# Optimization experiments

Measured on AMD Instinct MI355X. Metric: run time of the kernel, lower is better.

Reference implementation:

```python
import jax, jax.numpy as jnp
import numpy as np

B, N, K = 4, 40960, 16
D_IN, D_OUT = 32, 64


def setup_inputs() -> dict:
    key = jax.random.key(0)
    keys = iter(jax.random.split(key, 48))
    def nrm(shape, scale):
        return (jax.random.normal(next(keys), shape, jnp.float32) * scale).astype(jnp.float32)
    inp = {
        "feature": jax.random.normal(next(keys), (B, N, D_IN), jnp.float32),
        "xyz": jax.random.uniform(next(keys), (B, N, 3), jnp.float32),
        "neigh_idx": jax.random.randint(next(keys), (B, N, K), 0, N, jnp.int32),
    }
    def conv_bn(name, cin, cout):
        inp["w_" + name] = nrm((cin, cout), (2.0 / cin) ** 0.5)
        inp["s_" + name] = 1.0 + nrm((cout,), 0.1)  # folded BN scale: gamma/sqrt(var+eps)
        inp["b_" + name] = nrm((cout,), 0.1)        # folded BN bias: beta - mean*scale
    conv_bn("mlp1", D_IN, D_OUT // 2)
    conv_bn("lfa1", 10, D_OUT // 2)
    inp["w_att1_fc"] = nrm((D_OUT, D_OUT), (2.0 / D_OUT) ** 0.5)
    conv_bn("att1_mlp", D_OUT, D_OUT // 2)
    conv_bn("lfa2", D_OUT // 2, D_OUT // 2)
    inp["w_att2_fc"] = nrm((D_OUT, D_OUT), (2.0 / D_OUT) ** 0.5)
    conv_bn("att2_mlp", D_OUT, D_OUT)
    conv_bn("mlp2", D_OUT, 2 * D_OUT)
    conv_bn("sc", D_IN, 2 * D_OUT)
    return inp


def _gather(pc, idx):
    # pc: [B,N,D], idx: [B,N,K] -> [B,N,K,D]
    b, n, k = idx.shape
    flat = jnp.take_along_axis(pc, idx.reshape(b, n * k, 1), axis=1)
    return flat.reshape(b, n, k, pc.shape[-1])


def _cb(x, w, s, b, relu=True):
    # 1x1 conv + folded BN (+ ReLU), channels-last
    y = jnp.einsum('...i,io->...o', x, w) * s + b
    return jnp.maximum(y, 0.0) if relu else y


def _att_pool(fs, w_fc, w, s, b):
    # fs: [B,N,K,C]; softmax-attention pooling over K, then mlp
    scores = jax.nn.softmax(jnp.einsum('bnkc,cd->bnkd', fs, w_fc), axis=2)
    agg = jnp.sum(fs * scores, axis=2)  # [B,N,C]
    return _cb(agg, w, s, b)


def _rel_pos(xyz, idx):
    nbr = _gather(xyz, idx)                           # [B,N,K,3]
    tile = jnp.broadcast_to(xyz[:, :, None, :], nbr.shape)
    rel = tile - nbr
    dist = jnp.sqrt(jnp.sum(rel * rel, axis=-1, keepdims=True))
    return jnp.concatenate([dist, rel, tile, nbr], axis=-1)  # [B,N,K,10]


def reference(feature, xyz, neigh_idx,
              w_mlp1, s_mlp1, b_mlp1,
              w_lfa1, s_lfa1, b_lfa1,
              w_att1_fc, w_att1_mlp, s_att1_mlp, b_att1_mlp,
              w_lfa2, s_lfa2, b_lfa2,
              w_att2_fc, w_att2_mlp, s_att2_mlp, b_att2_mlp,
              w_mlp2, s_mlp2, b_mlp2,
              w_sc, s_sc, b_sc):
    f_pc = _cb(feature, w_mlp1, s_mlp1, b_mlp1)                   # [B,N,d/2]
    f_xyz = _cb(_rel_pos(xyz, neigh_idx), w_lfa1, s_lfa1, b_lfa1)  # [B,N,K,d/2]
    f_nb = _gather(f_pc, neigh_idx)                                # [B,N,K,d/2]
    f_agg = _att_pool(jnp.concatenate([f_nb, f_xyz], axis=-1),
                      w_att1_fc, w_att1_mlp, s_att1_mlp, b_att1_mlp)  # [B,N,d/2]
    f_xyz2 = _cb(f_xyz, w_lfa2, s_lfa2, b_lfa2)                    # [B,N,K,d/2]
    f_nb2 = _gather(f_agg, neigh_idx)                              # [B,N,K,d/2]
    f_pc2 = _att_pool(jnp.concatenate([f_nb2, f_xyz2], axis=-1),
                      w_att2_fc, w_att2_mlp, s_att2_mlp, b_att2_mlp)  # [B,N,d]
    out = _cb(f_pc2, w_mlp2, s_mlp2, b_mlp2, relu=False)           # [B,N,2d]
    sc = _cb(feature, w_sc, s_sc, b_sc, relu=False)
    return jax.nn.leaky_relu(out + sc, negative_slope=0.2)
```

## Files before the change

kernel.cpp:

```cpp
#include <hip/hip_runtime.h>
#include <hip/hip_bf16.h>

#define NPTS  40960
#define BNPTS 163840
#define KNB   16

#define PK_MLP1 0
#define PK_FC1  1280
#define PK_FC2  6912
#define PK_L1   12544
#define PK_L2   13824
#define PK_M1   15104
#define PK_M2   17920
#define PK_W2   23552
#define PK_WS   34816
#define PK_TOTAL 39936

using bf16x8 = __attribute__((ext_vector_type(8))) short;
using f32x4  = __attribute__((ext_vector_type(4))) float;

__device__ __forceinline__ unsigned short f2bf(float x) {
    union { float f; unsigned u; } v; v.f = x;
    unsigned r = v.u + 0x7fffu + ((v.u >> 16) & 1u);
    return (unsigned short)(r >> 16);
}
__device__ __forceinline__ float bf2f(unsigned short u) {
    union { unsigned u; float f; } v; v.u = ((unsigned)u) << 16;
    return v.f;
}
__device__ __forceinline__ unsigned pk2(float lo, float hi) {
    union { __hip_bfloat162 h; unsigned u; } v;
    v.h = __float22bfloat162_rn(float2{lo, hi});
    return v.u;
}
__device__ __forceinline__ bf16x8 pack8(float a0, float a1, float a2, float a3,
                                        float a4, float a5, float a6, float a7) {
    union { unsigned u[4]; bf16x8 v; } w;
    w.u[0] = pk2(a0, a1); w.u[1] = pk2(a2, a3);
    w.u[2] = pk2(a4, a5); w.u[3] = pk2(a6, a7);
    return w.v;
}
__device__ __forceinline__ f32x4 mfma16(bf16x8 a, bf16x8 b, f32x4 c) {
    return __builtin_amdgcn_mfma_f32_16x16x32_bf16(a, b, c, 0, 0, 0);
}
__device__ __forceinline__ float exp2_fast(float x) { return __builtin_amdgcn_exp2f(x); }
__device__ __forceinline__ float rcp_fast(float x)  { return __builtin_amdgcn_rcpf(x); }

__global__ __launch_bounds__(256)
void k_prep(const float* __restrict__ wm1, const float* __restrict__ wfc1,
            const float* __restrict__ wfc2,
            const float* __restrict__ wlfa1, const float* __restrict__ slfa1, const float* __restrict__ blfa1,
            const float* __restrict__ wlfa2,
            const float* __restrict__ wam1, const float* __restrict__ wam2,
            const float* __restrict__ w2, const float* __restrict__ wsc,
            unsigned short* __restrict__ pk)
{
    const int tid = threadIdx.x, blk = blockIdx.x;
    const float LOG2E = 1.4426950408889634f;
    switch (blk) {
    case 0:
        for (int t = tid; t < 32 * 32; t += 256) {
            int c = t >> 5, d = t & 31;
            pk[PK_MLP1 + d * 40 + c] = f2bf(wm1[t]);
        }
        break;
    case 1:
        for (int t = tid; t < 64 * 64; t += 256) {
            int c = t >> 6, d = t & 63;
            pk[PK_FC1 + d * 88 + c] = f2bf(wfc1[t] * LOG2E);
        }
        break;
    case 2:
        for (int t = tid; t < 64 * 64; t += 256) {
            int c = t >> 6, d = t & 63;
            pk[PK_FC2 + d * 88 + c] = f2bf(wfc2[t] * LOG2E);
        }
        break;
    case 3:
        for (int t = tid; t < 32 * 32; t += 256) {
            int k = t >> 5, d = t & 31;
            int slot = (d & 1) * 16 + (d >> 1);
            float v1 = k < 10 ? wlfa1[k * 32 + d] * slfa1[d] : (k == 10 ? blfa1[d] : 0.f);
            pk[PK_L1 + slot * 40 + k] = f2bf(v1);
            pk[PK_L2 + slot * 40 + k] = f2bf(wlfa2[k * 32 + d]);
        }
        break;
    case 4:
        for (int t = tid; t < 64 * 32; t += 256) {
            int c = t / 32, d = t % 32;
            int slot = (d & 1) * 16 + (d >> 1);
            pk[PK_M1 + slot * 88 + c] = f2bf(wam1[t]);
        }
        break;
    case 5:
        for (int t = tid; t < 64 * 64; t += 256) {
            int c = t >> 6, d = t & 63;
            int slot = (d >> 5) * 32 + (d & 1) * 16 + ((d & 31) >> 1);
            pk[PK_M2 + slot * 88 + c] = f2bf(wam2[t]);
        }
        break;
    case 6:
        for (int t = tid; t < 64 * 128; t += 256) {
            int c = t >> 7, d = t & 127;
            pk[PK_W2 + d * 88 + c] = f2bf(w2[t]);
        }
        break;
    case 7:
        for (int t = tid; t < 32 * 128; t += 256) {
            int c = t >> 7, d = t & 127;
            pk[PK_WS + d * 40 + c] = f2bf(wsc[t]);
        }
        break;
    }
}

__global__ __launch_bounds__(256)
void k_mlp1(const float* __restrict__ feature, const unsigned short* __restrict__ pk,
            const float* __restrict__ s, const float* __restrict__ b,
            unsigned short* __restrict__ f_pc)
{
    const int tid = threadIdx.x;
    const int lid = tid & 63, wv = tid >> 6;
    const int col = lid & 15, quad = lid >> 4;
    bf16x8 B0 = *(const bf16x8*)&pk[PK_MLP1 + col * 40 + quad * 8];
    bf16x8 B1 = *(const bf16x8*)&pk[PK_MLP1 + (16 + col) * 40 + quad * 8];
    float s0 = s[col], b0 = b[col], s1 = s[16 + col], b1 = b[16 + col];
    for (int itp = 0; itp < 4; itp++) {
        const int p0 = blockIdx.x * 256 + wv * 64 + itp * 16;
        const float* fr = &feature[(size_t)(p0 + col) * 32 + quad * 8];
        float4 u0 = *(const float4*)fr;
        float4 u1 = *(const float4*)(fr + 4);
        bf16x8 a = pack8(u0.x, u0.y, u0.z, u0.w, u1.x, u1.y, u1.z, u1.w);
        f32x4 z = {0.f, 0.f, 0.f, 0.f};
        f32x4 d0 = mfma16(a, B0, z);
        f32x4 d1 = mfma16(a, B1, z);
        #pragma unroll
        for (int r = 0; r < 4; r++) {
            int p = p0 + quad * 4 + r;
            f_pc[(size_t)p * 32 + col]      = f2bf(fmaxf(d0[r] * s0 + b0, 0.f));
            f_pc[(size_t)p * 32 + 16 + col] = f2bf(fmaxf(d1[r] * s1 + b1, 0.f));
        }
    }
}

template<int NOUT, bool HAS_LFA2>
__global__ __launch_bounds__(256, 4)
void k_att(const float* __restrict__ xyz, const int* __restrict__ nidx,
           const unsigned short* __restrict__ src,
           const unsigned short* __restrict__ wl1T, const unsigned short* __restrict__ wl2T,
           const float* __restrict__ slfa2, const float* __restrict__ blfa2,
           const unsigned short* __restrict__ wfcT, const unsigned short* __restrict__ wmT,
           const float* __restrict__ smlp, const float* __restrict__ bmlp,
           unsigned short* __restrict__ out)
{
    constexpr int NP = NOUT / 32;
    constexpr int WS = 88;
    __shared__ __align__(16) char smem[16384];
    char* uni = smem;

    const int tid = threadIdx.x;
    const int lid = tid & 63, wv = tid >> 6;
    const int col = lid & 15, quad = lid >> 4;

    bf16x8 Bfc[4][2];
    #pragma unroll
    for (int nt = 0; nt < 4; nt++)
        #pragma unroll
        for (int ks = 0; ks < 2; ks++)
            Bfc[nt][ks] = *(const bf16x8*)&wfcT[(nt * 16 + col) * WS + ks * 32 + quad * 8];
    bf16x8 Bl1e = *(const bf16x8*)&wl1T[col * 40 + quad * 8];
    bf16x8 Bl1o = *(const bf16x8*)&wl1T[(16 + col) * 40 + quad * 8];
    bf16x8 Bl2e{}, Bl2o{};
    float sl2e = 0.f, bl2e = 0.f, sl2o = 0.f, bl2o = 0.f;
    if (HAS_LFA2) {
        Bl2e = *(const bf16x8*)&wl2T[col * 40 + quad * 8];
        Bl2o = *(const bf16x8*)&wl2T[(16 + col) * 40 + quad * 8];
        sl2e = slfa2[2 * col]; bl2e = blfa2[2 * col];
        sl2o = slfa2[2 * col + 1]; bl2o = blfa2[2 * col + 1];
    }
    float sme[NP], bme[NP], smo[NP], bmo[NP];
    #pragma unroll
    for (int tp = 0; tp < NP; tp++) {
        sme[tp] = smlp[tp * 32 + 2 * col]; bme[tp] = bmlp[tp * 32 + 2 * col];
        smo[tp] = smlp[tp * 32 + 2 * col + 1]; bmo[tp] = bmlp[tp * 32 + 2 * col + 1];
    }
    bf16x8 Bme_r[2], Bmo_r[2];
    if constexpr (NOUT == 32) {
        #pragma unroll
        for (int ks = 0; ks < 2; ks++) {
            Bme_r[ks] = *(const bf16x8*)&wmT[col * WS + ks * 32 + quad * 8];
            Bmo_r[ks] = *(const bf16x8*)&wmT[(16 + col) * WS + ks * 32 + quad * 8];
        }
    }

    unsigned short* fc  = (unsigned short*)(uni) + wv * (16 * WS);
    unsigned short* ag  = (unsigned short*)(uni + 11264) + wv * (4 * 72);
    unsigned short* nb  = (unsigned short*)(uni + 13568) + wv * 256;
    float*          cxy = (float*)(uni + 15616) + wv * 48;

    const int blk = (int)blockIdx.x;
    const int vblk = (blk & 7) * 320 + (blk >> 3);
    const int pbase = vblk * 64 + wv * 16;
    const int pb = (pbase / NPTS) * NPTS;
    const unsigned short* srcb = src + (size_t)pb * 32;
    const float* xyzb = xyz + (size_t)pb * 3;

    {
        int4 t4 = *(const int4*)&nidx[(size_t)pbase * KNB + lid * 4];
        ushort4 u = make_ushort4((unsigned short)t4.x, (unsigned short)t4.y,
                                 (unsigned short)t4.z, (unsigned short)t4.w);
        *(ushort4*)&nb[lid * 4] = u;
        if (lid < 48) cxy[lid] = xyz[(size_t)pbase * 3 + lid];
    }

    const f32x4 z = {0.f, 0.f, 0.f, 0.f};
    bf16x8 vs; float nx = 0.f, ny = 0.f, nz = 0.f;
    {
        int j = (int)nb[col];
        vs = *(const bf16x8*)(srcb + (size_t)j * 32 + quad * 8);
        if (quad < 2) { const float* xp = xyzb + (size_t)j * 3; nx = xp[0]; ny = xp[1]; nz = xp[2]; }
    }

    #pragma unroll 1
    for (int it = 0; it < 16; it++) {
        const int p = pbase + it;
        bf16x8 a0 = vs;
        *(bf16x8*)&fc[col * WS + quad * 8] = a0;

        float cx = cxy[it * 3], cy = cxy[it * 3 + 1], cz = cxy[it * 3 + 2];
        float rx = cx - nx, ry = cy - ny, rz = cz - nz;
        float dd = sqrtf(rx * rx + ry * ry + rz * rz);
        float f0 = 0.f, f1 = 0.f, f2 = 0.f, f3 = 0.f, f4 = 0.f, f5 = 0.f, f6 = 0.f, f7 = 0.f;
        if (quad == 0)      { f0 = dd; f1 = rx; f2 = ry; f3 = rz; f4 = cx; f5 = cy; f6 = cz; f7 = nx; }
        else if (quad == 1) { f0 = ny; f1 = nz; f2 = 1.0f; }
        bf16x8 al = pack8(f0, f1, f2, f3, f4, f5, f6, f7);

        {
            int itn = it < 15 ? it + 1 : 15;
            int j = (int)nb[itn * 16 + col];
            vs = *(const bf16x8*)(srcb + (size_t)j * 32 + quad * 8);
            if (quad < 2) { const float* xp = xyzb + (size_t)j * 3; nx = xp[0]; ny = xp[1]; nz = xp[2]; }
        }

        {
            f32x4 d0 = mfma16(al, Bl1e, z);
            f32x4 d1 = mfma16(al, Bl1o, z);
            #pragma unroll
            for (int r = 0; r < 4; r++) {
                float ye = fmaxf(d0[r], 0.f);
                float yo = fmaxf(d1[r], 0.f);
                *(unsigned*)&fc[(quad * 4 + r) * WS + 32 + 2 * col] = pk2(ye, yo);
            }
            if (HAS_LFA2) {
                bf16x8 a2 = *(const bf16x8*)&fc[col * WS + 32 + quad * 8];
                f32x4 e0 = mfma16(a2, Bl2e, z);
                f32x4 e1 = mfma16(a2, Bl2o, z);
                #pragma unroll
                for (int r = 0; r < 4; r++) {
                    float ye = fmaxf(e0[r] * sl2e + bl2e, 0.f);
                    float yo = fmaxf(e1[r] * sl2o + bl2o, 0.f);
                    *(unsigned*)&fc[(quad * 4 + r) * WS + 32 + 2 * col] = pk2(ye, yo);
                }
            }
        }

        {
            bf16x8 a1 = *(const bf16x8*)&fc[col * WS + 32 + quad * 8];
            #pragma unroll
            for (int nt = 0; nt < 4; nt++) {
                f32x4 L = mfma16(a1, Bfc[nt][1], mfma16(a0, Bfc[nt][0], z));
                float e0 = exp2_fast(L[0]), e1 = exp2_fast(L[1]);
                float e2 = exp2_fast(L[2]), e3 = exp2_fast(L[3]);
                float sden = (e0 + e1) + (e2 + e3);
                const unsigned short* frr = &fc[quad * 4 * WS + nt * 16 + col];
                float av = e0 * bf2f(frr[0]) + e1 * bf2f(frr[WS]) + e2 * bf2f(frr[2 * WS]) + e3 * bf2f(frr[3 * WS]);
                av   += __shfl_xor(av, 16, 64);
                sden += __shfl_xor(sden, 16, 64);
                av   += __shfl_xor(av, 32, 64);
                sden += __shfl_xor(sden, 32, 64);
                if (quad == 0) ag[(it & 3) * 72 + nt * 16 + col] = f2bf(av * rcp_fast(sden));
            }
        }

        if ((it & 3) == 3) {
            bf16x8 am0 = *(const bf16x8*)&ag[(col & 3) * 72 + quad * 8];
            bf16x8 am1 = *(const bf16x8*)&ag[(col & 3) * 72 + 32 + quad * 8];
            #pragma unroll
            for (int tp = 0; tp < NP; tp++) {
                bf16x8 Be0, Be1, Bo0, Bo1;
                if constexpr (NOUT == 32) {
                    Be0 = Bme_r[0]; Be1 = Bme_r[1];
                    Bo0 = Bmo_r[0]; Bo1 = Bmo_r[1];
                } else {
                    Be0 = *(const bf16x8*)&wmT[(tp * 32 + col) * WS + quad * 8];
                    Be1 = *(const bf16x8*)&wmT[(tp * 32 + col) * WS + 32 + quad * 8];
                    Bo0 = *(const bf16x8*)&wmT[(tp * 32 + 16 + col) * WS + quad * 8];
                    Bo1 = *(const bf16x8*)&wmT[(tp * 32 + 16 + col) * WS + 32 + quad * 8];
                }
                f32x4 de = mfma16(am1, Be1, mfma16(am0, Be0, z));
                f32x4 dq = mfma16(am1, Bo1, mfma16(am0, Bo0, z));
                if (quad == 0) {
                    #pragma unroll
                    for (int r = 0; r < 4; r++) {
                        float ye = fmaxf(de[r] * sme[tp] + bme[tp], 0.f);
                        float yo = fmaxf(dq[r] * smo[tp] + bmo[tp], 0.f);
                        *(unsigned*)&out[(size_t)(p - 3 + r) * NOUT + tp * 32 + 2 * col] = pk2(ye, yo);
                    }
                }
            }
        }
    }
}

__global__ __launch_bounds__(256)
void k_out(const unsigned short* __restrict__ f_pc2, const float* __restrict__ feature,
           const unsigned short* __restrict__ pk,
           const float* __restrict__ s2, const float* __restrict__ b2,
           const float* __restrict__ ssc, const float* __restrict__ bsc,
           float* __restrict__ out)
{
    __shared__ float sA[128], sB2[128], sC[128];
    const int tid = threadIdx.x;
    if (tid < 128) { sA[tid] = s2[tid]; sB2[tid] = ssc[tid]; sC[tid] = b2[tid] + bsc[tid]; }
    __syncthreads();
    const int lid = tid & 63, wv = tid >> 6;
    const int col = lid & 15, quad = lid >> 4;
    const unsigned short* w2T = pk + PK_W2;
    const unsigned short* wsT = pk + PK_WS;
    const f32x4 z = {0.f, 0.f, 0.f, 0.f};
    #pragma unroll 1
    for (int itp = 0; itp < 2; itp++) {
        const int p0 = blockIdx.x * 128 + wv * 32 + itp * 16;
        const unsigned short* ar = &f_pc2[(size_t)(p0 + col) * 64 + quad * 8];
        bf16x8 a10 = *(const bf16x8*)ar;
        bf16x8 a11 = *(const bf16x8*)(ar + 32);
        const float* fr = &feature[(size_t)(p0 + col) * 32 + quad * 8];
        float4 u0 = *(const float4*)fr;
        float4 u1 = *(const float4*)(fr + 4);
        bf16x8 a2 = pack8(u0.x, u0.y, u0.z, u0.w, u1.x, u1.y, u1.z, u1.w);
        #pragma unroll 2
        for (int nt = 0; nt < 8; nt++) {
            bf16x8 bk0 = *(const bf16x8*)&w2T[(nt * 16 + col) * 88 + quad * 8];
            bf16x8 bk1 = *(const bf16x8*)&w2T[(nt * 16 + col) * 88 + 32 + quad * 8];
            bf16x8 bs  = *(const bf16x8*)&wsT[(nt * 16 + col) * 40 + quad * 8];
            f32x4 d = mfma16(a11, bk1, mfma16(a10, bk0, z));
            f32x4 e = mfma16(a2, bs, z);
            int n = nt * 16 + col;
            float ss = sA[n], st = sB2[n], bb = sC[n];
            #pragma unroll
            for (int r = 0; r < 4; r++) {
                float y = d[r] * ss + e[r] * st + bb;
                y = y > 0.f ? y : 0.2f * y;
                out[(size_t)(p0 + quad * 4 + r) * 128 + n] = y;
            }
        }
    }
}

extern "C" void kernel_launch(void* const* d_in, const int* in_sizes, int n_in,
                              void* d_out, int out_size, void* d_ws, size_t ws_size,
                              hipStream_t stream) {
    const float* feature = (const float*)d_in[0];
    const float* xyz     = (const float*)d_in[1];
    const int*   nidx    = (const int*)d_in[2];
    const float* w_mlp1 = (const float*)d_in[3];
    const float* s_mlp1 = (const float*)d_in[4];
    const float* b_mlp1 = (const float*)d_in[5];
    const float* w_lfa1 = (const float*)d_in[6];
    const float* s_lfa1 = (const float*)d_in[7];
    const float* b_lfa1 = (const float*)d_in[8];
    const float* w_att1_fc  = (const float*)d_in[9];
    const float* w_att1_mlp = (const float*)d_in[10];
    const float* s_att1_mlp = (const float*)d_in[11];
    const float* b_att1_mlp = (const float*)d_in[12];
    const float* w_lfa2 = (const float*)d_in[13];
    const float* s_lfa2 = (const float*)d_in[14];
    const float* b_lfa2 = (const float*)d_in[15];
    const float* w_att2_fc  = (const float*)d_in[16];
    const float* w_att2_mlp = (const float*)d_in[17];
    const float* s_att2_mlp = (const float*)d_in[18];
    const float* b_att2_mlp = (const float*)d_in[19];
    const float* w_mlp2 = (const float*)d_in[20];
    const float* s_mlp2 = (const float*)d_in[21];
    const float* b_mlp2 = (const float*)d_in[22];
    const float* w_sc = (const float*)d_in[23];
    const float* s_sc = (const float*)d_in[24];
    const float* b_sc = (const float*)d_in[25];

    unsigned short* f_pc  = (unsigned short*)d_ws;
    unsigned short* f_agg = f_pc  + (size_t)BNPTS * 32;
    unsigned short* f_pc2 = f_agg + (size_t)BNPTS * 32;
    unsigned short* pkw   = f_pc2 + (size_t)BNPTS * 64;
    float* out = (float*)d_out;

    k_prep<<<8, 256, 0, stream>>>(w_mlp1, w_att1_fc, w_att2_fc,
                                  w_lfa1, s_lfa1, b_lfa1, w_lfa2,
                                  w_att1_mlp, w_att2_mlp, w_mlp2, w_sc, pkw);
    k_mlp1<<<BNPTS / 256, 256, 0, stream>>>(feature, pkw, s_mlp1, b_mlp1, f_pc);
    k_att<32, false><<<BNPTS / 64, 256, 0, stream>>>(
        xyz, nidx, f_pc,
        pkw + PK_L1, pkw + PK_L1,
        s_lfa1, b_lfa1,
        pkw + PK_FC1, pkw + PK_M1, s_att1_mlp, b_att1_mlp, f_agg);
    k_att<64, true><<<BNPTS / 64, 256, 0, stream>>>(
        xyz, nidx, f_agg,
        pkw + PK_L1, pkw + PK_L2,
        s_lfa2, b_lfa2,
        pkw + PK_FC2, pkw + PK_M2, s_att2_mlp, b_att2_mlp, f_pc2);
    k_out<<<BNPTS / 128, 256, 0, stream>>>(
        f_pc2, feature, pkw,
        s_mlp2, b_mlp2, s_sc, b_sc, out);
}
```

Baseline: 364.7 us.

## Interleave weight columns for paired stores and double-buffer attention LDS tile

Repacks the mlp1, mlp2 and shortcut weights so each lane computes an adjacent even/odd output pair. This lets k_mlp1 write packed 32-bit bf16 pairs and k_out write float2 stores instead of scalar ones, and it moves k_out's scale/bias from shared memory into registers. k_att now double-buffers its per-wave fc LDS tile across iterations and unrolls by two, aiming to overlap consecutive iterations. The cost is more LDS per block (27 KB instead of 16 KB), which may lower occupancy, plus more registers.

```diff
diff --git a/kernel.cpp b/kernel.cpp
--- a/kernel.cpp
+++ b/kernel.cpp
@@ -61,7 +61,8 @@
     case 0:
         for (int t = tid; t < 32 * 32; t += 256) {
             int c = t >> 5, d = t & 31;
-            pk[PK_MLP1 + d * 40 + c] = f2bf(wm1[t]);
+            int slot = (d & 1) * 16 + (d >> 1);
+            pk[PK_MLP1 + slot * 40 + c] = f2bf(wm1[t]);
         }
         break;
     case 1:
@@ -102,13 +103,15 @@
     case 6:
         for (int t = tid; t < 64 * 128; t += 256) {
             int c = t >> 7, d = t & 127;
-            pk[PK_W2 + d * 88 + c] = f2bf(w2[t]);
+            int slot = (d >> 5) * 32 + (d & 1) * 16 + ((d & 31) >> 1);
+            pk[PK_W2 + slot * 88 + c] = f2bf(w2[t]);
         }
         break;
     case 7:
         for (int t = tid; t < 32 * 128; t += 256) {
             int c = t >> 7, d = t & 127;
-            pk[PK_WS + d * 40 + c] = f2bf(wsc[t]);
+            int slot = (d >> 5) * 32 + (d & 1) * 16 + ((d & 31) >> 1);
+            pk[PK_WS + slot * 40 + c] = f2bf(wsc[t]);
         }
         break;
     }
@@ -124,7 +127,7 @@
     const int col = lid & 15, quad = lid >> 4;
     bf16x8 B0 = *(const bf16x8*)&pk[PK_MLP1 + col * 40 + quad * 8];
     bf16x8 B1 = *(const bf16x8*)&pk[PK_MLP1 + (16 + col) * 40 + quad * 8];
-    float s0 = s[col], b0 = b[col], s1 = s[16 + col], b1 = b[16 + col];
+    float s0 = s[2 * col], b0 = b[2 * col], s1 = s[2 * col + 1], b1 = b[2 * col + 1];
     for (int itp = 0; itp < 4; itp++) {
         const int p0 = blockIdx.x * 256 + wv * 64 + itp * 16;
         const float* fr = &feature[(size_t)(p0 + col) * 32 + quad * 8];
@@ -137,8 +140,9 @@
         #pragma unroll
         for (int r = 0; r < 4; r++) {
             int p = p0 + quad * 4 + r;
-            f_pc[(size_t)p * 32 + col]      = f2bf(fmaxf(d0[r] * s0 + b0, 0.f));
-            f_pc[(size_t)p * 32 + 16 + col] = f2bf(fmaxf(d1[r] * s1 + b1, 0.f));
+            float ye = fmaxf(d0[r] * s0 + b0, 0.f);
+            float yo = fmaxf(d1[r] * s1 + b1, 0.f);
+            *(unsigned*)&f_pc[(size_t)p * 32 + 2 * col] = pk2(ye, yo);
         }
     }
 }
@@ -155,7 +159,7 @@
 {
     constexpr int NP = NOUT / 32;
     constexpr int WS = 88;
-    __shared__ __align__(16) char smem[16384];
+    __shared__ __align__(16) char smem[27648];
     char* uni = smem;
 
     const int tid = threadIdx.x;
@@ -193,10 +197,10 @@
         }
     }
 
-    unsigned short* fc  = (unsigned short*)(uni) + wv * (16 * WS);
-    unsigned short* ag  = (unsigned short*)(uni + 11264) + wv * (4 * 72);
-    unsigned short* nb  = (unsigned short*)(uni + 13568) + wv * 256;
-    float*          cxy = (float*)(uni + 15616) + wv * 48;
+    unsigned short* fc  = (unsigned short*)(uni) + wv * 2816;
+    unsigned short* ag  = (unsigned short*)(uni + 22528) + wv * 288;
+    unsigned short* nb  = (unsigned short*)(uni + 24832) + wv * 256;
+    float*          cxy = (float*)(uni + 26880) + wv * 48;
 
     const int blk = (int)blockIdx.x;
     const int vblk = (blk & 7) * 320 + (blk >> 3);
@@ -221,11 +225,12 @@
         if (quad < 2) { const float* xp = xyzb + (size_t)j * 3; nx = xp[0]; ny = xp[1]; nz = xp[2]; }
     }
 
-    #pragma unroll 1
+    #pragma unroll 2
     for (int it = 0; it < 16; it++) {
         const int p = pbase + it;
+        unsigned short* fcb = fc + (it & 1) * 1408;
         bf16x8 a0 = vs;
-        *(bf16x8*)&fc[col * WS + quad * 8] = a0;
+        *(bf16x8*)&fcb[col * WS + quad * 8] = a0;
 
         float cx = cxy[it * 3], cy = cxy[it * 3 + 1], cz = cxy[it * 3 + 2];
         float rx = cx - nx, ry = cy - ny, rz = cz - nz;
@@ -249,30 +254,30 @@
             for (int r = 0; r < 4; r++) {
                 float ye = fmaxf(d0[r], 0.f);
                 float yo = fmaxf(d1[r], 0.f);
-                *(unsigned*)&fc[(quad * 4 + r) * WS + 32 + 2 * col] = pk2(ye, yo);
+                *(unsigned*)&fcb[(quad * 4 + r) * WS + 32 + 2 * col] = pk2(ye, yo);
             }
             if (HAS_LFA2) {
-                bf16x8 a2 = *(const bf16x8*)&fc[col * WS + 32 + quad * 8];
+                bf16x8 a2 = *(const bf16x8*)&fcb[col * WS + 32 + quad * 8];
                 f32x4 e0 = mfma16(a2, Bl2e, z);
                 f32x4 e1 = mfma16(a2, Bl2o, z);
                 #pragma unroll
                 for (int r = 0; r < 4; r++) {
                     float ye = fmaxf(e0[r] * sl2e + bl2e, 0.f);
                     float yo = fmaxf(e1[r] * sl2o + bl2o, 0.f);
-                    *(unsigned*)&fc[(quad * 4 + r) * WS + 32 + 2 * col] = pk2(ye, yo);
+                    *(unsigned*)&fcb[(quad * 4 + r) * WS + 32 + 2 * col] = pk2(ye, yo);
                 }
             }
         }
 
         {
-            bf16x8 a1 = *(const bf16x8*)&fc[col * WS + 32 + quad * 8];
+            bf16x8 a1 = *(const bf16x8*)&fcb[col * WS + 32 + quad * 8];
             #pragma unroll
             for (int nt = 0; nt < 4; nt++) {
                 f32x4 L = mfma16(a1, Bfc[nt][1], mfma16(a0, Bfc[nt][0], z));
                 float e0 = exp2_fast(L[0]), e1 = exp2_fast(L[1]);
                 float e2 = exp2_fast(L[2]), e3 = exp2_fast(L[3]);
                 float sden = (e0 + e1) + (e2 + e3);
-                const unsigned short* frr = &fc[quad * 4 * WS + nt * 16 + col];
+                const unsigned short* frr = &fcb[quad * 4 * WS + nt * 16 + col];
                 float av = e0 * bf2f(frr[0]) + e1 * bf2f(frr[WS]) + e2 * bf2f(frr[2 * WS]) + e3 * bf2f(frr[3 * WS]);
                 av   += __shfl_xor(av, 16, 64);
                 sden += __shfl_xor(sden, 16, 64);
@@ -319,14 +324,19 @@
            const float* __restrict__ ssc, const float* __restrict__ bsc,
            float* __restrict__ out)
 {
-    __shared__ float sA[128], sB2[128], sC[128];
     const int tid = threadIdx.x;
-    if (tid < 128) { sA[tid] = s2[tid]; sB2[tid] = ssc[tid]; sC[tid] = b2[tid] + bsc[tid]; }
-    __syncthreads();
     const int lid = tid & 63, wv = tid >> 6;
     const int col = lid & 15, quad = lid >> 4;
     const unsigned short* w2T = pk + PK_W2;
     const unsigned short* wsT = pk + PK_WS;
+    float sse[4], sso[4], ste[4], sto[4], bbe[4], bbo[4];
+    #pragma unroll
+    for (int m = 0; m < 4; m++) {
+        int ce = m * 32 + 2 * col, co = ce + 1;
+        sse[m] = s2[ce]; sso[m] = s2[co];
+        ste[m] = ssc[ce]; sto[m] = ssc[co];
+        bbe[m] = b2[ce] + bsc[ce]; bbo[m] = b2[co] + bsc[co];
+    }
     const f32x4 z = {0.f, 0.f, 0.f, 0.f};
     #pragma unroll 1
     for (int itp = 0; itp < 2; itp++) {
@@ -338,20 +348,26 @@
         float4 u0 = *(const float4*)fr;
         float4 u1 = *(const float4*)(fr + 4);
         bf16x8 a2 = pack8(u0.x, u0.y, u0.z, u0.w, u1.x, u1.y, u1.z, u1.w);
-        #pragma unroll 2
-        for (int nt = 0; nt < 8; nt++) {
-            bf16x8 bk0 = *(const bf16x8*)&w2T[(nt * 16 + col) * 88 + quad * 8];
-            bf16x8 bk1 = *(const bf16x8*)&w2T[(nt * 16 + col) * 88 + 32 + quad * 8];
-            bf16x8 bs  = *(const bf16x8*)&wsT[(nt * 16 + col) * 40 + quad * 8];
-            f32x4 d = mfma16(a11, bk1, mfma16(a10, bk0, z));
-            f32x4 e = mfma16(a2, bs, z);
-            int n = nt * 16 + col;
-            float ss = sA[n], st = sB2[n], bb = sC[n];
+        #pragma unroll
+        for (int m = 0; m < 4; m++) {
+            bf16x8 ke0 = *(const bf16x8*)&w2T[(m * 32 + col) * 88 + quad * 8];
+            bf16x8 ke1 = *(const bf16x8*)&w2T[(m * 32 + col) * 88 + 32 + quad * 8];
+            bf16x8 ko0 = *(const bf16x8*)&w2T[(m * 32 + 16 + col) * 88 + quad * 8];
+            bf16x8 ko1 = *(const bf16x8*)&w2T[(m * 32 + 16 + col) * 88 + 32 + quad * 8];
+            bf16x8 se  = *(const bf16x8*)&wsT[(m * 32 + col) * 40 + quad * 8];
+            bf16x8 so  = *(const bf16x8*)&wsT[(m * 32 + 16 + col) * 40 + quad * 8];
+            f32x4 de = mfma16(a11, ke1, mfma16(a10, ke0, z));
+            f32x4 dq = mfma16(a11, ko1, mfma16(a10, ko0, z));
+            f32x4 ee = mfma16(a2, se, z);
+            f32x4 eo = mfma16(a2, so, z);
             #pragma unroll
             for (int r = 0; r < 4; r++) {
-                float y = d[r] * ss + e[r] * st + bb;
-                y = y > 0.f ? y : 0.2f * y;
-                out[(size_t)(p0 + quad * 4 + r) * 128 + n] = y;
+                float ye = de[r] * sse[m] + ee[r] * ste[m] + bbe[m];
+                float yo = dq[r] * sso[m] + eo[r] * sto[m] + bbo[m];
+                ye = ye > 0.f ? ye : 0.2f * ye;
+                yo = yo > 0.f ? yo : 0.2f * yo;
+                *(float2*)&out[(size_t)(p0 + quad * 4 + r) * 128 + m * 32 + 2 * col] =
+                    make_float2(ye, yo);
             }
         }
     }
```

After: 365.5 us. Within noise of the previous version (+0.2%).
